# Optimization experiments

Measured on AMD Instinct MI355X. Metric: run time of the kernel, lower is better.

Reference implementation:

```python
import jax, jax.numpy as jnp
import numpy as np


def setup_inputs() -> dict:
    key = jax.random.key(0)
    k1, k2, k3, k4 = jax.random.split(key, 4)
    N, C_in, C_out, H, W, K = 32, 128, 256, 56, 56, 3
    x = jax.random.normal(k1, (N, C_in, H, W), dtype=jnp.float32)
    # ternary weights in {-1, 0, +1}, stored as int8 like the torch buffer
    w_q = jax.random.randint(k2, (C_out, C_in, K, K), -1, 2).astype(jnp.int8)
    s = jax.random.uniform(k3, (C_out, 1, 1), dtype=jnp.float32) + 0.5
    bias = jax.random.normal(k4, (C_out,), dtype=jnp.float32)
    return {"x": x, "w_q": w_q, "s": s, "bias": bias}


def reference(x, w_q, s, bias):
    # y = conv2d(x, w_q.float()) * s + bias, stride=1, padding=1, dilation=1, groups=1
    w = w_q.astype(x.dtype)  # ternary {-1,0,+1} cast to float, as in torch
    y = jax.lax.conv_general_dilated(
        x, w,
        window_strides=(1, 1),
        padding=((1, 1), (1, 1)),
        lhs_dilation=(1, 1),
        rhs_dilation=(1, 1),
        dimension_numbers=("NCHW", "OIHW", "NCHW"),
        feature_group_count=1,
    )
    y = y * s  # s: [C_out,1,1] broadcasts over [N,C_out,H,W]
    y = y + bias.reshape(1, -1, 1, 1)
    return y
```

## Files before the change

### kernel.cpp

```cpp
#include <hip/hip_runtime.h>
#include <hip/hip_bf16.h>

typedef unsigned short ushort_t;

#define N_IMG 32
#define C_IN  128
#define C_OUT 256
#define H_SZ  56
#define W_SZ  56
#define HW_SZ (H_SZ * W_SZ)
#define K_TOT (C_IN * 9)
#define WP 64
#define HP 58
#define ROW_E (WP * C_IN)

typedef __attribute__((ext_vector_type(8))) short bf16x8;
typedef __attribute__((ext_vector_type(4))) float floatx4;

__device__ __forceinline__ void gl_lds16(const ushort_t* g, ushort_t* l) {
  __builtin_amdgcn_global_load_lds(
      (const __attribute__((address_space(1))) void*)g,
      (__attribute__((address_space(3))) void*)l, 16, 0, 0);
}

__device__ __forceinline__ ushort_t f2bf(float f) {
  __hip_bfloat16 b = __float2bfloat16(f);
  return *reinterpret_cast<ushort_t*>(&b);
}

__global__ void wtrans_kernel(const int* __restrict__ wq, ushort_t* __restrict__ wt) {
  int idx = blockIdx.x * 256 + threadIdx.x;
  if (idx >= C_OUT * K_TOT) return;
  int co = idx / K_TOT;
  int k  = idx - co * K_TOT;
  int tap = k >> 7;
  int c   = k & 127;
  int kh = tap / 3, kw = tap - kh * 3;
  int v = wq[((co * C_IN + c) * 3 + kh) * 3 + kw];
  wt[idx] = f2bf((float)v);
}

__global__ __launch_bounds__(256) void xpad_kernel(const float* __restrict__ x,
                                                   ushort_t* __restrict__ xp) {
  int b = blockIdx.x;
  int t = threadIdx.x;
  ushort_t* row = xp + (size_t)b * ROW_E;
  int n = b / HP;
  int h1 = b - n * HP;
  if (b >= N_IMG * HP || h1 == 0 || h1 == HP - 1) {
    uint4 z = {0u, 0u, 0u, 0u};
    uint4* r4 = (uint4*)row;
#pragma unroll
    for (int i = 0; i < 4; ++i) r4[i * 256 + t] = z;
    return;
  }
  __shared__ float tile[C_IN * 57];
  int h = h1 - 1;
  const float* xb = x + (size_t)n * C_IN * HW_SZ + h * W_SZ;
#pragma unroll
  for (int i = 0; i < 7; ++i) {
    int idx = i * 256 + t;
    int c = idx / 14, f = idx - c * 14;
    float4 v = *(const float4*)(xb + (size_t)c * HW_SZ + f * 4);
    float* dst = &tile[c * 57 + f * 4];
    dst[0] = v.x; dst[1] = v.y; dst[2] = v.z; dst[3] = v.w;
  }
  __syncthreads();
  unsigned int* r32 = (unsigned int*)row;
#pragma unroll
  for (int i = 0; i < 16; ++i) {
    int idx = i * 256 + t;
    int wp = idx >> 6, cp = idx & 63;
    unsigned int u = 0;
    if (wp >= 1 && wp <= W_SZ) {
      int w = wp - 1;
      u = (unsigned int)f2bf(tile[(2 * cp) * 57 + w]) |
          ((unsigned int)f2bf(tile[(2 * cp + 1) * 57 + w]) << 16);
    }
    r32[wp * 64 + cp] = u;
  }
}

__global__ __launch_bounds__(256) void bitconv_kernel(
    const ushort_t* __restrict__ wt, const ushort_t* __restrict__ xp,
    const float* __restrict__ s, const float* __restrict__ bias,
    float* __restrict__ out) {
  __shared__ ushort_t As[2][128 * 32];
  __shared__ ushort_t Bs[2][128 * 32];

  int d = blockIdx.x;
  int xcd = d & 7;
  int r   = d >> 3;
  int co0 = (r & 1) * 128;
  int sp_tile = xcd * 112 + (r >> 1);
  int nh0 = sp_tile * 2;
  int n  = nh0 / H_SZ;
  int hh = nh0 - n * H_SZ;

  int tid  = threadIdx.x;
  int lane = tid & 63;
  int wid  = tid >> 6;
  int l15  = lane & 15;
  int quad = lane >> 4;
  int wave_m = (wid >> 1) * 64;
  int wave_n = (wid & 1) * 64;
  int lrow = lane >> 2;
  int lchk = (lane & 3) * 8;

  const ushort_t* a_src[2];
  const ushort_t* b_src[2];
  int dst_off[2];
#pragma unroll
  for (int g = 0; g < 2; ++g) {
    int rrow = wid * 32 + g * 16 + lrow;
    a_src[g] = wt + (size_t)(co0 + rrow) * K_TOT + lchk;
    int hrow = rrow >> 6, wpp = (rrow & 63) + 1;
    b_src[g] = xp + (size_t)((n * HP + hh + 1 + hrow) * WP + wpp) * C_IN + lchk;
    dst_off[g] = (wid * 32 + g * 16) * 32;
  }

  floatx4 acc[4][4];
#pragma unroll
  for (int mi = 0; mi < 4; ++mi)
#pragma unroll
    for (int ni = 0; ni < 4; ++ni)
      acc[mi][ni] = (floatx4){0.f, 0.f, 0.f, 0.f};

  auto stage = [&](int st, int buf) {
    int tap = st >> 2;
    int c0  = (st & 3) << 5;
    int kh  = tap / 3;
    int kw  = tap - kh * 3;
    int aoff = tap * C_IN + c0;
    int boff = (kh - 1) * ROW_E + (kw - 1) * C_IN + c0;
#pragma unroll
    for (int g = 0; g < 2; ++g) {
      gl_lds16(a_src[g] + aoff, &As[buf][dst_off[g]]);
      gl_lds16(b_src[g] + boff, &Bs[buf][dst_off[g]]);
    }
  };

  stage(0, 0);
  int cur = 0;
  for (int st = 0; st < 36; ++st) {
    if (st < 35) {
      stage(st + 1, cur ^ 1);
      asm volatile("s_waitcnt vmcnt(4)" ::: "memory");
    } else {
      asm volatile("s_waitcnt vmcnt(0)" ::: "memory");
    }
    __builtin_amdgcn_s_barrier();

    bf16x8 af[4], bfv[4];
#pragma unroll
    for (int mi = 0; mi < 4; ++mi)
      af[mi] = *(const bf16x8*)&As[cur][(wave_m + mi * 16 + l15) * 32 + quad * 8];
#pragma unroll
    for (int ni = 0; ni < 4; ++ni)
      bfv[ni] = *(const bf16x8*)&Bs[cur][(wave_n + ni * 16 + l15) * 32 + quad * 8];
#pragma unroll
    for (int mi = 0; mi < 4; ++mi)
#pragma unroll
      for (int ni = 0; ni < 4; ++ni)
        acc[mi][ni] = __builtin_amdgcn_mfma_f32_16x16x32_bf16(
            af[mi], bfv[ni], acc[mi][ni], 0, 0, 0);

    __builtin_amdgcn_s_barrier();
    cur ^= 1;
  }

  int h_out = hh + (wid & 1);
#pragma unroll
  for (int mi = 0; mi < 4; ++mi) {
#pragma unroll
    for (int rg = 0; rg < 4; ++rg) {
      int co = co0 + wave_m + mi * 16 + quad * 4 + rg;
      float sv = s[co];
      float bv = bias[co];
      float* ob = out + (size_t)(n * C_OUT + co) * HW_SZ + h_out * W_SZ;
#pragma unroll
      for (int ni = 0; ni < 4; ++ni) {
        int wpp = ni * 16 + l15;
        if (wpp < W_SZ)
          ob[wpp] = acc[mi][ni][rg] * sv + bv;
      }
    }
  }
}

extern "C" void kernel_launch(void* const* d_in, const int* in_sizes, int n_in,
                              void* d_out, int out_size, void* d_ws, size_t ws_size,
                              hipStream_t stream) {
  const float* x    = (const float*)d_in[0];
  const int*   wq   = (const int*)d_in[1];
  const float* s    = (const float*)d_in[2];
  const float* bias = (const float*)d_in[3];
  float* out = (float*)d_out;

  char* ws = (char*)d_ws;
  ushort_t* wt = (ushort_t*)ws;
  ushort_t* xp = (ushort_t*)(ws + 589824);

  hipLaunchKernelGGL(wtrans_kernel, dim3((C_OUT * K_TOT) / 256), dim3(256), 0, stream,
                     wq, wt);
  hipLaunchKernelGGL(xpad_kernel, dim3(N_IMG * HP + 1), dim3(256), 0, stream, x, xp);
  hipLaunchKernelGGL(bitconv_kernel, dim3(1792), dim3(256), 0, stream,
                     wt, xp, s, bias, out);
}
```

Before: 236.9 us.

## Double K-tile depth to 64 with XOR-swizzled LDS layout and unrolled main loop

Each pipeline stage now loads a 64-wide K slice instead of 32, halving the number of stages and barriers (18 instead of 36). The LDS tiles are laid out with an XOR swizzle on the 16-byte chunk index so the wider 128-byte rows do not cause bank conflicts on MFMA operand reads. The main loop is fully unrolled. The cost is doubled LDS use per block (64 KB), which may lower occupancy, and more in-flight loads per stage.

```diff
diff --git a/kernel.cpp b/kernel.cpp
--- a/kernel.cpp
+++ b/kernel.cpp
@@ -85,8 +85,8 @@
     const ushort_t* __restrict__ wt, const ushort_t* __restrict__ xp,
     const float* __restrict__ s, const float* __restrict__ bias,
     float* __restrict__ out) {
-  __shared__ ushort_t As[2][128 * 32];
-  __shared__ ushort_t Bs[2][128 * 32];
+  __shared__ ushort_t As[2][128 * 64];
+  __shared__ ushort_t Bs[2][128 * 64];
 
   int d = blockIdx.x;
   int xcd = d & 7;
@@ -104,20 +104,22 @@
   int quad = lane >> 4;
   int wave_m = (wid >> 1) * 64;
   int wave_n = (wid & 1) * 64;
-  int lrow = lane >> 2;
-  int lchk = (lane & 3) * 8;
-
-  const ushort_t* a_src[2];
-  const ushort_t* b_src[2];
-  int dst_off[2];
-#pragma unroll
-  for (int g = 0; g < 2; ++g) {
-    int rrow = wid * 32 + g * 16 + lrow;
-    a_src[g] = wt + (size_t)(co0 + rrow) * K_TOT + lchk;
+
+  int qoff = (((lane & 7) ^ (lane >> 3)) * 8);
+  const ushort_t* a_src[4];
+  const ushort_t* b_src[4];
+  int dst_e[4];
+#pragma unroll
+  for (int g = 0; g < 4; ++g) {
+    int rrow = wid * 32 + g * 8 + (lane >> 3);
+    a_src[g] = wt + (size_t)(co0 + rrow) * K_TOT + qoff;
     int hrow = rrow >> 6, wpp = (rrow & 63) + 1;
-    b_src[g] = xp + (size_t)((n * HP + hh + 1 + hrow) * WP + wpp) * C_IN + lchk;
-    dst_off[g] = (wid * 32 + g * 16) * 32;
-  }
+    b_src[g] = xp + (size_t)((n * HP + hh + 1 + hrow) * WP + wpp) * C_IN + qoff;
+    dst_e[g] = (wid * 32 + g * 8) * 64;
+  }
+
+  int koff0 = (quad ^ (l15 & 7)) * 8;
+  int koff1 = koff0 ^ 32;
 
   floatx4 acc[4][4];
 #pragma unroll
@@ -126,47 +128,50 @@
     for (int ni = 0; ni < 4; ++ni)
       acc[mi][ni] = (floatx4){0.f, 0.f, 0.f, 0.f};
 
-  auto stage = [&](int st, int buf) {
-    int tap = st >> 2;
-    int c0  = (st & 3) << 5;
-    int kh  = tap / 3;
-    int kw  = tap - kh * 3;
-    int aoff = tap * C_IN + c0;
-    int boff = (kh - 1) * ROW_E + (kw - 1) * C_IN + c0;
-#pragma unroll
-    for (int g = 0; g < 2; ++g) {
-      gl_lds16(a_src[g] + aoff, &As[buf][dst_off[g]]);
-      gl_lds16(b_src[g] + boff, &Bs[buf][dst_off[g]]);
+  auto stage = [&](int tap, int half, int buf) {
+    int aoff = tap * C_IN + half * 64;
+    int boff = (tap / 3 - 1) * ROW_E + (tap % 3 - 1) * C_IN + half * 64;
+#pragma unroll
+    for (int g = 0; g < 4; ++g) {
+      gl_lds16(a_src[g] + aoff, &As[buf][dst_e[g]]);
+      gl_lds16(b_src[g] + boff, &Bs[buf][dst_e[g]]);
     }
   };
 
-  stage(0, 0);
-  int cur = 0;
-  for (int st = 0; st < 36; ++st) {
-    if (st < 35) {
-      stage(st + 1, cur ^ 1);
-      asm volatile("s_waitcnt vmcnt(4)" ::: "memory");
+  stage(0, 0, 0);
+#pragma unroll
+  for (int st = 0; st < 18; ++st) {
+    int buf = st & 1;
+    if (st < 17) {
+      stage((st + 1) >> 1, (st + 1) & 1, buf ^ 1);
+      asm volatile("s_waitcnt vmcnt(8)" ::: "memory");
     } else {
       asm volatile("s_waitcnt vmcnt(0)" ::: "memory");
     }
     __builtin_amdgcn_s_barrier();
-
-    bf16x8 af[4], bfv[4];
-#pragma unroll
-    for (int mi = 0; mi < 4; ++mi)
-      af[mi] = *(const bf16x8*)&As[cur][(wave_m + mi * 16 + l15) * 32 + quad * 8];
-#pragma unroll
-    for (int ni = 0; ni < 4; ++ni)
-      bfv[ni] = *(const bf16x8*)&Bs[cur][(wave_n + ni * 16 + l15) * 32 + quad * 8];
-#pragma unroll
-    for (int mi = 0; mi < 4; ++mi)
+    asm volatile("" ::: "memory");
+
+#pragma unroll
+    for (int ks = 0; ks < 2; ++ks) {
+      int ko = ks ? koff1 : koff0;
+      bf16x8 af[4], bfv[4];
+#pragma unroll
+      for (int mi = 0; mi < 4; ++mi)
+        af[mi] = *(const bf16x8*)&As[buf][(wave_m + mi * 16 + l15) * 64 + ko];
 #pragma unroll
       for (int ni = 0; ni < 4; ++ni)
-        acc[mi][ni] = __builtin_amdgcn_mfma_f32_16x16x32_bf16(
-            af[mi], bfv[ni], acc[mi][ni], 0, 0, 0);
-
+        bfv[ni] = *(const bf16x8*)&Bs[buf][(wave_n + ni * 16 + l15) * 64 + ko];
+#pragma unroll
+      for (int mi = 0; mi < 4; ++mi)
+#pragma unroll
+        for (int ni = 0; ni < 4; ++ni)
+          acc[mi][ni] = __builtin_amdgcn_mfma_f32_16x16x32_bf16(
+              af[mi], bfv[ni], acc[mi][ni], 0, 0, 0);
+    }
+
+    asm volatile("" ::: "memory");
     __builtin_amdgcn_s_barrier();
-    cur ^= 1;
+    asm volatile("" ::: "memory");
   }
 
   int h_out = hh + (wid & 1);
```

Measured after the change: 216.7 us. -8.5%, faster.

## Triple-buffer LDS stages with one barrier and XOR-swizzle LDS layout

Applied to the files above, without the earlier changes.

Moves the GEMM main loop from double to triple buffering. Loads are issued two stages ahead and the trailing barrier is dropped, leaving a single barrier per iteration. The 16-byte chunks within each 32-element LDS row are also XOR-swizzled on both the global-to-LDS write and the fragment read, to cut LDS bank conflicts. LDS use rises to 48KB per block, which may reduce occupancy, and the loop is fully unrolled.

```diff
diff --git a/kernel.cpp b/kernel.cpp
--- a/kernel.cpp
+++ b/kernel.cpp
@@ -85,8 +85,8 @@
     const ushort_t* __restrict__ wt, const ushort_t* __restrict__ xp,
     const float* __restrict__ s, const float* __restrict__ bias,
     float* __restrict__ out) {
-  __shared__ ushort_t As[2][128 * 32];
-  __shared__ ushort_t Bs[2][128 * 32];
+  __shared__ ushort_t As[3][128 * 32];
+  __shared__ ushort_t Bs[3][128 * 32];
 
   int d = blockIdx.x;
   int xcd = d & 7;
@@ -104,20 +104,21 @@
   int quad = lane >> 4;
   int wave_m = (wid >> 1) * 64;
   int wave_n = (wid & 1) * 64;
-  int lrow = lane >> 2;
-  int lchk = (lane & 3) * 8;
-
+
+  int qoff = (((lane & 3) ^ ((lane >> 3) & 3)) * 8);
   const ushort_t* a_src[2];
   const ushort_t* b_src[2];
-  int dst_off[2];
+  int dst_e[2];
 #pragma unroll
   for (int g = 0; g < 2; ++g) {
-    int rrow = wid * 32 + g * 16 + lrow;
-    a_src[g] = wt + (size_t)(co0 + rrow) * K_TOT + lchk;
+    int rrow = wid * 32 + g * 16 + (lane >> 2);
+    a_src[g] = wt + (size_t)(co0 + rrow) * K_TOT + qoff;
     int hrow = rrow >> 6, wpp = (rrow & 63) + 1;
-    b_src[g] = xp + (size_t)((n * HP + hh + 1 + hrow) * WP + wpp) * C_IN + lchk;
-    dst_off[g] = (wid * 32 + g * 16) * 32;
-  }
+    b_src[g] = xp + (size_t)((n * HP + hh + 1 + hrow) * WP + wpp) * C_IN + qoff;
+    dst_e[g] = (wid * 32 + g * 16) * 32;
+  }
+
+  int koff = (quad ^ ((l15 >> 1) & 3)) * 8;
 
   floatx4 acc[4][4];
 #pragma unroll
@@ -128,45 +129,47 @@
 
   auto stage = [&](int st, int buf) {
     int tap = st >> 2;
-    int c0  = (st & 3) << 5;
-    int kh  = tap / 3;
-    int kw  = tap - kh * 3;
-    int aoff = tap * C_IN + c0;
-    int boff = (kh - 1) * ROW_E + (kw - 1) * C_IN + c0;
+    int q32 = st & 3;
+    int aoff = tap * C_IN + q32 * 32;
+    int boff = (tap / 3 - 1) * ROW_E + (tap % 3 - 1) * C_IN + q32 * 32;
 #pragma unroll
     for (int g = 0; g < 2; ++g) {
-      gl_lds16(a_src[g] + aoff, &As[buf][dst_off[g]]);
-      gl_lds16(b_src[g] + boff, &Bs[buf][dst_off[g]]);
+      gl_lds16(a_src[g] + aoff, &As[buf][dst_e[g]]);
+      gl_lds16(b_src[g] + boff, &Bs[buf][dst_e[g]]);
     }
   };
 
   stage(0, 0);
-  int cur = 0;
+  stage(1, 1);
+#pragma unroll
   for (int st = 0; st < 36; ++st) {
-    if (st < 35) {
-      stage(st + 1, cur ^ 1);
+    if (st < 34) {
+      asm volatile("s_waitcnt vmcnt(4)" ::: "memory");
+    } else if (st == 34) {
       asm volatile("s_waitcnt vmcnt(4)" ::: "memory");
     } else {
       asm volatile("s_waitcnt vmcnt(0)" ::: "memory");
     }
     __builtin_amdgcn_s_barrier();
-
+    asm volatile("" ::: "memory");
+
+    if (st < 34)
+      stage(st + 2, (st + 2) % 3);
+
+    int buf = st % 3;
     bf16x8 af[4], bfv[4];
 #pragma unroll
     for (int mi = 0; mi < 4; ++mi)
-      af[mi] = *(const bf16x8*)&As[cur][(wave_m + mi * 16 + l15) * 32 + quad * 8];
+      af[mi] = *(const bf16x8*)&As[buf][(wave_m + mi * 16 + l15) * 32 + koff];
 #pragma unroll
     for (int ni = 0; ni < 4; ++ni)
-      bfv[ni] = *(const bf16x8*)&Bs[cur][(wave_n + ni * 16 + l15) * 32 + quad * 8];
+      bfv[ni] = *(const bf16x8*)&Bs[buf][(wave_n + ni * 16 + l15) * 32 + koff];
 #pragma unroll
     for (int mi = 0; mi < 4; ++mi)
 #pragma unroll
       for (int ni = 0; ni < 4; ++ni)
         acc[mi][ni] = __builtin_amdgcn_mfma_f32_16x16x32_bf16(
             af[mi], bfv[ni], acc[mi][ni], 0, 0, 0);
-
-    __builtin_amdgcn_s_barrier();
-    cur ^= 1;
   }
 
   int h_out = hh + (wid & 1);
```

Result: faster. 227.3 us (-4.0%).
